# Performance work log

Measured on AMD Instinct MI355X. Metric: run time of the kernel, lower is better.

Reference implementation:

```python
import jax, jax.numpy as jnp
import numpy as np

GROUPS = 32
EPS = 1e-5
N_HEADS = 8


def setup_inputs() -> dict:
    key = jax.random.key(0)
    ks = jax.random.split(key, 12)
    B, H, W, C = 16, 64, 64, 512
    Nctx, Dctx = 77, 768
    s_c = 1.0 / np.sqrt(C)
    s_ctx = 1.0 / np.sqrt(Dctx)
    return {
        "x": jax.random.normal(ks[0], (B, H, W, C), jnp.float32),
        "context": jax.random.normal(ks[1], (B, Nctx, Dctx), jnp.float32),
        "gn_scale": jnp.ones((C,), jnp.float32),
        "gn_bias": jnp.zeros((C,), jnp.float32),
        "wq": jax.random.normal(ks[2], (C, C), jnp.float32) * s_c,
        "bq": jnp.zeros((C,), jnp.float32),
        "wk": jax.random.normal(ks[3], (Dctx, C), jnp.float32) * s_ctx,
        "bk": jnp.zeros((C,), jnp.float32),
        "wv": jax.random.normal(ks[4], (Dctx, C), jnp.float32) * s_ctx,
        "bv": jnp.zeros((C,), jnp.float32),
        "wo": jax.random.normal(ks[5], (C, C), jnp.float32) * s_c,
        "bo": jnp.zeros((C,), jnp.float32),
    }


def _group_norm(x, scale, bias):
    B, H, W, C = x.shape
    xg = x.reshape(B, H, W, GROUPS, C // GROUPS)
    mean = jnp.mean(xg, axis=(1, 2, 4), keepdims=True)
    var = jnp.var(xg, axis=(1, 2, 4), keepdims=True)
    xn = (xg - mean) * jax.lax.rsqrt(var + EPS)
    return xn.reshape(B, H, W, C) * scale + bias


def reference(x, context, gn_scale, gn_bias, wq, bq, wk, bk, wv, bv, wo, bo):
    B, H, W, C = x.shape
    head_dim = C // N_HEADS
    h = _group_norm(x, gn_scale, gn_bias)
    h_flat = h.reshape(B, H * W, C)
    Q = h_flat @ wq + bq                      # [B, N, C]
    K = context @ wk + bk                     # [B, Nctx, C]
    V = context @ wv + bv

    def split_heads(t):
        b, n, c = t.shape
        return t.reshape(b, n, N_HEADS, head_dim).transpose(0, 2, 1, 3)

    Qh, Kh, Vh = split_heads(Q), split_heads(K), split_heads(V)
    scale = 1.0 / jnp.sqrt(jnp.asarray(head_dim, x.dtype))
    scores = jnp.einsum('bhid,bhjd->bhij', Qh, Kh) * scale
    attn = jax.nn.softmax(scores, axis=-1)
    out = jnp.einsum('bhij,bhjd->bhid', attn, Vh)  # [B, h, N, d]
    out = out.transpose(0, 2, 1, 3).reshape(B, H * W, C)
    out = out @ wo + bo
    return out.reshape(B, H, W, C) + x
```

## Files before the change

### kernel.cpp

```cpp
#include <hip/hip_runtime.h>
#include <hip/hip_bf16.h>

typedef __attribute__((ext_vector_type(4))) float f32x4;
typedef __attribute__((ext_vector_type(8))) short bf16x8;
typedef unsigned short u16;

#define AS1 __attribute__((address_space(1)))
#define AS3 __attribute__((address_space(3)))

#define B_    16
#define HW_   4096
#define C_    512
#define NCTX  77
#define DCTX  768
#define NH    8
#define HD    64
#define EPSV  1e-5f

__device__ inline u16 f2bf(float f) {
    union { float f; unsigned u; } v; v.f = f;
    unsigned r = v.u + 0x7fffu + ((v.u >> 16) & 1u);
    return (u16)(r >> 16);
}
__device__ inline float bf2f(u16 h) {
    union { unsigned u; float f; } v; v.u = ((unsigned)h) << 16;
    return v.f;
}

__global__ __launch_bounds__(256) void gn_stats(const float* __restrict__ x,
                                                float* __restrict__ mean,
                                                float* __restrict__ rstd) {
    int b = blockIdx.x >> 5, g = blockIdx.x & 31;
    const float* px = x + (size_t)b * HW_ * C_ + g * 16;
    float s = 0.f, ss = 0.f;
    for (int t = threadIdx.x; t < HW_ * 4; t += 256) {
        int hw = t >> 2, c4 = (t & 3) * 4;
        const float4 v = *(const float4*)(px + (size_t)hw * C_ + c4);
        s  += v.x + v.y + v.z + v.w;
        ss += v.x * v.x + v.y * v.y + v.z * v.z + v.w * v.w;
    }
    for (int off = 32; off; off >>= 1) { s += __shfl_xor(s, off); ss += __shfl_xor(ss, off); }
    __shared__ float red[2][4];
    int wv = threadIdx.x >> 6, lane = threadIdx.x & 63;
    if (lane == 0) { red[0][wv] = s; red[1][wv] = ss; }
    __syncthreads();
    if (threadIdx.x == 0) {
        float S = red[0][0] + red[0][1] + red[0][2] + red[0][3];
        float SS = red[1][0] + red[1][1] + red[1][2] + red[1][3];
        float mn = S / 65536.f;
        float var = SS / 65536.f - mn * mn;
        mean[blockIdx.x] = mn;
        rstd[blockIdx.x] = rsqrtf(var + EPSV);
    }
}

__global__ __launch_bounds__(256) void transpose_cast(const float* __restrict__ src,
                                                      u16* __restrict__ dst, int K) {
    int idx = blockIdx.x * 256 + threadIdx.x;
    if (idx >= K * 512) return;
    int k = idx >> 9, n = idx & 511;
    dst[(size_t)n * K + k] = f2bf(src[idx]);
}

__global__ __launch_bounds__(256) void gemm_small(const float* __restrict__ A,
                                                  const u16* __restrict__ Bt,
                                                  const float* __restrict__ bias,
                                                  u16* __restrict__ out,
                                                  int M, int K) {
    __shared__ __align__(16) u16 As[128][40];
    __shared__ __align__(16) u16 Bs[128][40];
    int tid = threadIdx.x, lane = tid & 63, wid = tid >> 6;
    int wm = wid >> 1, wn = wid & 1;
    int row0 = blockIdx.y * 128, col0 = blockIdx.x * 128;
    int q = lane >> 4, r16 = lane & 15;

    f32x4 acc[4][4];
#pragma unroll
    for (int i = 0; i < 4; i++)
#pragma unroll
        for (int j = 0; j < 4; j++) acc[i][j] = (f32x4){0.f, 0.f, 0.f, 0.f};

    for (int k0 = 0; k0 < K; k0 += 32) {
#pragma unroll
        for (int it = 0; it < 2; ++it) {
            int e = it * 256 + tid;
            int rr = e >> 2, kc = (e & 3) * 8;
            int ga = row0 + rr; if (ga > M - 1) ga = M - 1;
            float4 a0 = *(const float4*)(A + (size_t)ga * K + k0 + kc);
            float4 a1 = *(const float4*)(A + (size_t)ga * K + k0 + kc + 4);
            bf16x8 av;
            av[0] = (short)f2bf(a0.x); av[1] = (short)f2bf(a0.y);
            av[2] = (short)f2bf(a0.z); av[3] = (short)f2bf(a0.w);
            av[4] = (short)f2bf(a1.x); av[5] = (short)f2bf(a1.y);
            av[6] = (short)f2bf(a1.z); av[7] = (short)f2bf(a1.w);
            *(bf16x8*)&As[rr][kc] = av;
            int gb = col0 + rr;
            bf16x8 bv = *(const bf16x8*)(Bt + (size_t)gb * K + k0 + kc);
            *(bf16x8*)&Bs[rr][kc] = bv;
        }
        __syncthreads();
        bf16x8 afr[4], bfr[4];
#pragma unroll
        for (int mi = 0; mi < 4; mi++) afr[mi] = *(const bf16x8*)&As[wm * 64 + mi * 16 + r16][q * 8];
#pragma unroll
        for (int ni = 0; ni < 4; ni++) bfr[ni] = *(const bf16x8*)&Bs[wn * 64 + ni * 16 + r16][q * 8];
#pragma unroll
        for (int mi = 0; mi < 4; mi++)
#pragma unroll
            for (int ni = 0; ni < 4; ni++)
                acc[mi][ni] = __builtin_amdgcn_mfma_f32_16x16x32_bf16(afr[mi], bfr[ni], acc[mi][ni], 0, 0, 0);
        __syncthreads();
    }

#pragma unroll
    for (int mi = 0; mi < 4; mi++) {
#pragma unroll
        for (int rr = 0; rr < 4; rr++) {
            int grow = row0 + wm * 64 + mi * 16 + q * 4 + rr;
            if (grow >= M) continue;
#pragma unroll
            for (int ni = 0; ni < 4; ni++) {
                int gcol = col0 + wn * 64 + ni * 16 + r16;
                float v = acc[mi][ni][rr] + bias[gcol];
                out[(size_t)grow * 512 + gcol] = f2bf(v);
            }
        }
    }
}

__global__ __launch_bounds__(256, 2) void gemm_fusedq(const float* __restrict__ x,
                                                      const float* __restrict__ mean,
                                                      const float* __restrict__ rstd,
                                                      const float* __restrict__ gns,
                                                      const float* __restrict__ gnb,
                                                      const u16* __restrict__ Bt,
                                                      const float* __restrict__ bias,
                                                      u16* __restrict__ out) {
    constexpr int K = 512;
    __shared__ __align__(16) u16 LA[2][8192];
    __shared__ __align__(16) u16 LB[2][8192];
    int tid = threadIdx.x, lane = tid & 63, wid = tid >> 6;
    int wr = wid >> 1, wc = wid & 1;
    int q = lane >> 4, r16 = lane & 15;

    int orig = blockIdx.x;
    int wg = (orig & 7) * 256 + (orig >> 3);
    int bx = wg & 3, by = wg >> 2;
    int row0 = by * 128, col0 = bx * 128;

    int srow = tid >> 3;
    int schunk = (tid & 7) ^ (srow & 7);
    const u16* gB = Bt + (size_t)(col0 + srow) * K + schunk * 8;
    const int lo = tid * 8;

    int c8 = tid & 7;
    int rbase = (tid >> 3) * 4;
    const float* xb = x + (size_t)(row0 + rbase) * 512 + c8 * 8;
    int bg0 = (row0 >> 12) * 32;

    f32x4 acc[4][4];
#pragma unroll
    for (int i = 0; i < 4; i++)
#pragma unroll
        for (int j = 0; j < 4; j++) acc[i][j] = (f32x4){0.f, 0.f, 0.f, 0.f};

    float4 ar[8];
    float mn, rs;
    float4 s0v, s1v, b0v, b1v;

#define LOADA(kt) do { _Pragma("unroll")                                          \
    for (int i_ = 0; i_ < 4; ++i_) {                                              \
        ar[2 * i_]     = *(const float4*)(xb + (kt) * 64 + (size_t)i_ * 512);     \
        ar[2 * i_ + 1] = *(const float4*)(xb + (kt) * 64 + (size_t)i_ * 512 + 4); \
    } } while (0)

#define LOADP(kt) do { int c0_ = (kt) * 64 + c8 * 8; int bg_ = bg0 + (c0_ >> 4);  \
    mn = mean[bg_]; rs = rstd[bg_];                                               \
    s0v = *(const float4*)(gns + c0_); s1v = *(const float4*)(gns + c0_ + 4);     \
    b0v = *(const float4*)(gnb + c0_); b1v = *(const float4*)(gnb + c0_ + 4);     \
  } while (0)

#define WRITEA(nbuf) do {                                                         \
    float m2_[8], a2_[8];                                                         \
    m2_[0]=rs*s0v.x; m2_[1]=rs*s0v.y; m2_[2]=rs*s0v.z; m2_[3]=rs*s0v.w;           \
    m2_[4]=rs*s1v.x; m2_[5]=rs*s1v.y; m2_[6]=rs*s1v.z; m2_[7]=rs*s1v.w;           \
    a2_[0]=b0v.x-mn*m2_[0]; a2_[1]=b0v.y-mn*m2_[1];                               \
    a2_[2]=b0v.z-mn*m2_[2]; a2_[3]=b0v.w-mn*m2_[3];                               \
    a2_[4]=b1v.x-mn*m2_[4]; a2_[5]=b1v.y-mn*m2_[5];                               \
    a2_[6]=b1v.z-mn*m2_[6]; a2_[7]=b1v.w-mn*m2_[7];                               \
    _Pragma("unroll")                                                             \
    for (int i_ = 0; i_ < 4; ++i_) {                                              \
        int row_ = rbase + i_;                                                    \
        bf16x8 pk_;                                                               \
        pk_[0]=(short)f2bf(ar[2*i_].x  *m2_[0]+a2_[0]);                           \
        pk_[1]=(short)f2bf(ar[2*i_].y  *m2_[1]+a2_[1]);                           \
        pk_[2]=(short)f2bf(ar[2*i_].z  *m2_[2]+a2_[2]);                           \
        pk_[3]=(short)f2bf(ar[2*i_].w  *m2_[3]+a2_[3]);                           \
        pk_[4]=(short)f2bf(ar[2*i_+1].x*m2_[4]+a2_[4]);                           \
        pk_[5]=(short)f2bf(ar[2*i_+1].y*m2_[5]+a2_[5]);                           \
        pk_[6]=(short)f2bf(ar[2*i_+1].z*m2_[6]+a2_[6]);                           \
        pk_[7]=(short)f2bf(ar[2*i_+1].w*m2_[7]+a2_[7]);                           \
        *(bf16x8*)&LA[nbuf][row_ * 64 + ((c8 ^ (row_ & 7)) * 8)] = pk_;           \
    } } while (0)

#define STG_B(kt, s) __builtin_amdgcn_global_load_lds( \
        (const AS1 void*)(gB + (kt) * 64 + (size_t)((s) * 32) * K), \
        (AS3 void*)(&LB[(kt) & 1][(s) * 2048 + lo]), 16, 0, 0)

#define PHASE_(buf, h, ks) do {                                                            \
    bf16x8 afr[2], bfr[4];                                                                 \
    const int ch_ = (((ks) * 4 + q) ^ (r16 & 7)) * 8;                                      \
    _Pragma("unroll")                                                                      \
    for (int mi = 0; mi < 2; mi++)                                                         \
        afr[mi] = *(const bf16x8*)&LA[buf][(wr * 64 + ((h) * 2 + mi) * 16 + r16) * 64 + ch_]; \
    _Pragma("unroll")                                                                      \
    for (int ni = 0; ni < 4; ni++)                                                         \
        bfr[ni] = *(const bf16x8*)&LB[buf][(wc * 64 + ni * 16 + r16) * 64 + ch_];          \
    __builtin_amdgcn_s_setprio(1);                                                         \
    _Pragma("unroll")                                                                      \
    for (int mi = 0; mi < 2; mi++)                                                         \
      _Pragma("unroll")                                                                    \
      for (int ni = 0; ni < 4; ni++)                                                       \
        acc[(h) * 2 + mi][ni] =                                                            \
            __builtin_amdgcn_mfma_f32_16x16x32_bf16(afr[mi], bfr[ni], acc[(h) * 2 + mi][ni], 0, 0, 0); \
    __builtin_amdgcn_s_setprio(0);                                                         \
  } while (0)

    LOADA(0); LOADP(0);
    asm volatile("" ::: "memory");
    STG_B(0, 0); STG_B(0, 1); STG_B(0, 2); STG_B(0, 3);
    asm volatile("s_waitcnt vmcnt(4)" ::: "memory");
    WRITEA(0);
    asm volatile("s_waitcnt lgkmcnt(0)" ::: "memory");

#pragma unroll
    for (int t = 0; t < 7; ++t) {
        const int buf = t & 1;
        LOADA(t + 1); LOADP(t + 1);
        asm volatile("" ::: "memory");
        STG_B(t + 1, 0); STG_B(t + 1, 1); STG_B(t + 1, 2); STG_B(t + 1, 3);
        asm volatile("s_waitcnt vmcnt(18)" ::: "memory");
        __builtin_amdgcn_s_barrier();
        asm volatile("" ::: "memory");
        PHASE_(buf, 0, 0); PHASE_(buf, 1, 0); PHASE_(buf, 0, 1); PHASE_(buf, 1, 1);
        asm volatile("s_waitcnt vmcnt(4)" ::: "memory");
        WRITEA(buf ^ 1);
        asm volatile("s_waitcnt lgkmcnt(0)" ::: "memory");
        __builtin_amdgcn_s_barrier();
        asm volatile("" ::: "memory");
    }
    asm volatile("s_waitcnt vmcnt(0) lgkmcnt(0)" ::: "memory");
    __builtin_amdgcn_s_barrier();
    asm volatile("" ::: "memory");
    PHASE_(1, 0, 0); PHASE_(1, 1, 0); PHASE_(1, 0, 1); PHASE_(1, 1, 1);
#undef LOADA
#undef LOADP
#undef WRITEA
#undef STG_B
#undef PHASE_

#pragma unroll
    for (int mi = 0; mi < 4; mi++) {
#pragma unroll
        for (int rr = 0; rr < 4; rr++) {
            int grow = row0 + wr * 64 + mi * 16 + q * 4 + rr;
#pragma unroll
            for (int ni = 0; ni < 4; ni++) {
                int gcol = col0 + wc * 64 + ni * 16 + r16;
                float v = acc[mi][ni][rr] + bias[gcol];
                out[(size_t)grow * 512 + gcol] = f2bf(v);
            }
        }
    }
}

__global__ __launch_bounds__(256, 4) void gemm_ring(const u16* __restrict__ A,
                                                    const u16* __restrict__ Bt,
                                                    const float* __restrict__ bias,
                                                    const float* __restrict__ res,
                                                    float* __restrict__ out) {
    constexpr int K = 512;
    __shared__ __align__(16) u16 LA[2][4096];
    __shared__ __align__(16) u16 LB[2][4096];
    int tid = threadIdx.x, lane = tid & 63, wid = tid >> 6;
    int wr = wid >> 1, wc = wid & 1;
    int q = lane >> 4, r16 = lane & 15;

    int orig = blockIdx.x;
    int wg = (orig & 7) * 256 + (orig >> 3);
    int bx = wg & 3, by = wg >> 2;
    int row0 = by * 128, col0 = bx * 128;

    int srow = tid >> 2;
    int schunk = (tid & 3) ^ (srow & 3);
    const u16* gA = A + (size_t)(row0 + srow) * K + schunk * 8;
    const u16* gB = Bt + (size_t)(col0 + srow) * K + schunk * 8;
    const int lo = tid * 8;

    f32x4 acc[4][4];
#pragma unroll
    for (int i = 0; i < 4; i++)
#pragma unroll
        for (int j = 0; j < 4; j++) acc[i][j] = (f32x4){0.f, 0.f, 0.f, 0.f};

#define STG(kt) do { int sl_ = (kt) & 1;                                              \
    __builtin_amdgcn_global_load_lds((const AS1 void*)(gA + (kt) * 32),               \
                                     (AS3 void*)(&LA[sl_][lo]), 16, 0, 0);            \
    __builtin_amdgcn_global_load_lds((const AS1 void*)(gA + (kt) * 32 + (size_t)64 * K), \
                                     (AS3 void*)(&LA[sl_][2048 + lo]), 16, 0, 0);     \
    __builtin_amdgcn_global_load_lds((const AS1 void*)(gB + (kt) * 32),               \
                                     (AS3 void*)(&LB[sl_][lo]), 16, 0, 0);            \
    __builtin_amdgcn_global_load_lds((const AS1 void*)(gB + (kt) * 32 + (size_t)64 * K), \
                                     (AS3 void*)(&LB[sl_][2048 + lo]), 16, 0, 0);     \
  } while (0)

#define COMPUTE(sl) do {                                                              \
    bf16x8 afr[4], bfr[4];                                                            \
    const int ch_ = (q ^ (r16 & 3)) * 8;                                              \
    _Pragma("unroll")                                                                 \
    for (int mi = 0; mi < 4; mi++)                                                    \
        afr[mi] = *(const bf16x8*)&LA[sl][(wr * 64 + mi * 16 + r16) * 32 + ch_];      \
    _Pragma("unroll")                                                                 \
    for (int ni = 0; ni < 4; ni++)                                                    \
        bfr[ni] = *(const bf16x8*)&LB[sl][(wc * 64 + ni * 16 + r16) * 32 + ch_];      \
    __builtin_amdgcn_s_setprio(1);                                                    \
    _Pragma("unroll")                                                                 \
    for (int mi = 0; mi < 4; mi++)                                                    \
      _Pragma("unroll")                                                               \
      for (int ni = 0; ni < 4; ni++)                                                  \
        acc[mi][ni] = __builtin_amdgcn_mfma_f32_16x16x32_bf16(afr[mi], bfr[ni], acc[mi][ni], 0, 0, 0); \
    __builtin_amdgcn_s_setprio(0);                                                    \
  } while (0)

    STG(0);
#pragma unroll
    for (int t = 0; t < 15; ++t) {
        STG(t + 1);
        asm volatile("s_waitcnt vmcnt(4)" ::: "memory");
        asm volatile("s_barrier" ::: "memory");
        COMPUTE(t & 1);
        asm volatile("s_barrier" ::: "memory");
    }
    asm volatile("s_waitcnt vmcnt(0)" ::: "memory");
    asm volatile("s_barrier" ::: "memory");
    COMPUTE(1);
#undef STG
#undef COMPUTE

#pragma unroll
    for (int mi = 0; mi < 4; mi++) {
#pragma unroll
        for (int rr = 0; rr < 4; rr++) {
            int grow = row0 + wr * 64 + mi * 16 + q * 4 + rr;
#pragma unroll
            for (int ni = 0; ni < 4; ni++) {
                int gcol = col0 + wc * 64 + ni * 16 + r16;
                float v = acc[mi][ni][rr] + bias[gcol];
                size_t idx = (size_t)grow * 512 + gcol;
                out[idx] = v + res[idx];
            }
        }
    }
}

__global__ __launch_bounds__(256) void attn_mfma(const u16* __restrict__ Qb,
                                                 const u16* __restrict__ Kb,
                                                 const u16* __restrict__ Vb,
                                                 u16* __restrict__ Ob) {
    __shared__ __align__(16) u16 Ks[80][72];
    __shared__ __align__(16) u16 VT[64][104];
    __shared__ __align__(16) u16 Ps[64][104];
    int tid = threadIdx.x, lane = tid & 63, wv = tid >> 6;
    int q = lane >> 4, r16 = lane & 15;
    int tile0 = blockIdx.x * 16;
    int bh = blockIdx.y;
    int b = bh >> 3, h = bh & 7;

    {
        unsigned* p0 = (unsigned*)&Ks[0][0];
        for (int i = tid; i < 2880; i += 256) p0[i] = 0u;
        unsigned* p1 = (unsigned*)&VT[0][0];
        for (int i = tid; i < 3328; i += 256) p1[i] = 0u;
        unsigned* p2 = (unsigned*)&Ps[0][0];
        for (int i = tid; i < 3328; i += 256) p2[i] = 0u;
    }
    __syncthreads();

    size_t kvbase = ((size_t)b * NCTX) * C_ + h * HD;
    for (int c = tid; c < NCTX * 8; c += 256) {
        int j = c >> 3, d8 = (c & 7) * 8;
        *(bf16x8*)&Ks[j][d8] = *(const bf16x8*)(Kb + kvbase + (size_t)j * C_ + d8);
    }
    for (int t = tid; t < NCTX * 64; t += 256) {
        int j = t >> 6, d = t & 63;
        VT[d][j] = Vb[kvbase + (size_t)j * C_ + d];
    }
    __syncthreads();

    const size_t tstep = (size_t)64 * C_;
    const u16* qp = Qb + ((size_t)b * HW_ + wv * 16 + r16) * C_ + h * HD + q * 8;
    bool v4 = (r16 < NCTX - 64);

    bf16x8 qc0 = *(const bf16x8*)(qp + (size_t)tile0 * tstep);
    bf16x8 qc1 = *(const bf16x8*)(qp + (size_t)tile0 * tstep + 32);

    for (int it = 0; it < 16; ++it) {
        int tile = tile0 + it;
        bf16x8 qn0 = qc0, qn1 = qc1;
        if (it < 15) {
            qn0 = *(const bf16x8*)(qp + (size_t)(tile + 1) * tstep);
            qn1 = *(const bf16x8*)(qp + (size_t)(tile + 1) * tstep + 32);
        }

        f32x4 accs[5];
#pragma unroll
        for (int nt = 0; nt < 5; ++nt) accs[nt] = (f32x4){0.f, 0.f, 0.f, 0.f};
#pragma unroll
        for (int nt = 0; nt < 5; ++nt) {
            bf16x8 kf = *(const bf16x8*)&Ks[nt * 16 + r16][q * 8];
            accs[nt] = __builtin_amdgcn_mfma_f32_16x16x32_bf16(qc0, kf, accs[nt], 0, 0, 0);
        }
#pragma unroll
        for (int nt = 0; nt < 5; ++nt) {
            bf16x8 kf = *(const bf16x8*)&Ks[nt * 16 + r16][32 + q * 8];
            accs[nt] = __builtin_amdgcn_mfma_f32_16x16x32_bf16(qc1, kf, accs[nt], 0, 0, 0);
        }

#pragma unroll
        for (int r = 0; r < 4; ++r) {
            float s[5];
#pragma unroll
            for (int nt = 0; nt < 5; ++nt) s[nt] = accs[nt][r] * 0.125f;
            float m = fmaxf(fmaxf(fmaxf(s[0], s[1]), fmaxf(s[2], s[3])), v4 ? s[4] : -3.0e38f);
#pragma unroll
            for (int off = 1; off < 16; off <<= 1) m = fmaxf(m, __shfl_xor(m, off));
            float e[5], sum = 0.f;
#pragma unroll
            for (int nt = 0; nt < 5; ++nt) {
                e[nt] = (nt < 4 || v4) ? __expf(s[nt] - m) : 0.f;
                sum += e[nt];
            }
#pragma unroll
            for (int off = 1; off < 16; off <<= 1) sum += __shfl_xor(sum, off);
            float inv = 1.0f / sum;
            int prow = wv * 16 + q * 4 + r;
#pragma unroll
            for (int nt = 0; nt < 5; ++nt)
                Ps[prow][nt * 16 + r16] = f2bf(e[nt] * inv);
        }

        f32x4 acco[4];
#pragma unroll
        for (int nt = 0; nt < 4; ++nt) acco[nt] = (f32x4){0.f, 0.f, 0.f, 0.f};
#pragma unroll
        for (int ks = 0; ks < 3; ++ks) {
            bf16x8 pf = *(const bf16x8*)&Ps[wv * 16 + r16][ks * 32 + q * 8];
#pragma unroll
            for (int nt = 0; nt < 4; ++nt) {
                bf16x8 vf = *(const bf16x8*)&VT[nt * 16 + r16][ks * 32 + q * 8];
                acco[nt] = __builtin_amdgcn_mfma_f32_16x16x32_bf16(pf, vf, acco[nt], 0, 0, 0);
            }
        }

        int row0 = tile * 64 + wv * 16;
#pragma unroll
        for (int nt = 0; nt < 4; ++nt)
#pragma unroll
            for (int r = 0; r < 4; ++r) {
                int row = row0 + q * 4 + r;
                int col = h * HD + nt * 16 + r16;
                Ob[((size_t)b * HW_ + row) * C_ + col] = f2bf(acco[nt][r]);
            }
        qc0 = qn0; qc1 = qn1;
    }
}

extern "C" void kernel_launch(void* const* d_in, const int* in_sizes, int n_in,
                              void* d_out, int out_size, void* d_ws, size_t ws_size,
                              hipStream_t stream) {
    const float* x   = (const float*)d_in[0];
    const float* ctx = (const float*)d_in[1];
    const float* gns = (const float*)d_in[2];
    const float* gnb = (const float*)d_in[3];
    const float* wq  = (const float*)d_in[4];
    const float* bq  = (const float*)d_in[5];
    const float* wk  = (const float*)d_in[6];
    const float* bk  = (const float*)d_in[7];
    const float* wv  = (const float*)d_in[8];
    const float* bv  = (const float*)d_in[9];
    const float* wo  = (const float*)d_in[10];
    const float* bo  = (const float*)d_in[11];

    char* ws = (char*)d_ws;
    float* mean = (float*)(ws + 0);
    float* rstd = (float*)(ws + 2048);
    u16* wqT  = (u16*)(ws + 4096);
    u16* wkT  = (u16*)(ws + 528384);
    u16* wvT  = (u16*)(ws + 1314816);
    u16* woT  = (u16*)(ws + 2101248);
    u16* aob  = (u16*)(ws + 4517888);
    u16* qb   = (u16*)(ws + 71626752);
    u16* kb   = (u16*)(ws + 138735616);
    u16* vb   = (u16*)(ws + 139997184);

    gn_stats<<<512, 256, 0, stream>>>(x, mean, rstd);
    transpose_cast<<<1024, 256, 0, stream>>>(wq, wqT, 512);
    transpose_cast<<<1536, 256, 0, stream>>>(wk, wkT, 768);
    transpose_cast<<<1536, 256, 0, stream>>>(wv, wvT, 768);
    transpose_cast<<<1024, 256, 0, stream>>>(wo, woT, 512);

    gemm_fusedq<<<2048, 256, 0, stream>>>(x, mean, rstd, gns, gnb, wqT, bq, qb);
    gemm_small<<<dim3(4, 10), 256, 0, stream>>>(ctx, wkT, bk, kb, 1232, 768);
    gemm_small<<<dim3(4, 10), 256, 0, stream>>>(ctx, wvT, bv, vb, 1232, 768);

    attn_mfma<<<dim3(4, 128), 256, 0, stream>>>(qb, kb, vb, aob);

    gemm_ring<<<2048, 256, 0, stream>>>(aob, woT, bo, x, (float*)d_out);
}
```

Baseline: 321.5 us.

## Merge weight transposes and K/V GEMMs into single launches; double attention grid

Folds the four weight transpose-cast launches into one kernel and the separate K and V projection GEMMs into one launch that picks K or V weights by block column. The attention kernel now processes 8 query tiles per block instead of 16, doubling the grid to 1024 blocks so more CUs have work. This cuts launch overhead and small-kernel tail time. In exchange, K/V staging into shared memory is repeated across twice as many blocks.

```diff
diff --git a/kernel.cpp b/kernel.cpp
--- a/kernel.cpp
+++ b/kernel.cpp
@@ -54,24 +54,50 @@
     }
 }
 
-__global__ __launch_bounds__(256) void transpose_cast(const float* __restrict__ src,
-                                                      u16* __restrict__ dst, int K) {
+__global__ __launch_bounds__(256) void transpose_all(const float* __restrict__ wq,
+                                                     const float* __restrict__ wk,
+                                                     const float* __restrict__ wv,
+                                                     const float* __restrict__ wo,
+                                                     u16* __restrict__ wqT,
+                                                     u16* __restrict__ wkT,
+                                                     u16* __restrict__ wvT,
+                                                     u16* __restrict__ woT) {
     int idx = blockIdx.x * 256 + threadIdx.x;
-    if (idx >= K * 512) return;
-    int k = idx >> 9, n = idx & 511;
-    dst[(size_t)n * K + k] = f2bf(src[idx]);
-}
-
-__global__ __launch_bounds__(256) void gemm_small(const float* __restrict__ A,
-                                                  const u16* __restrict__ Bt,
-                                                  const float* __restrict__ bias,
-                                                  u16* __restrict__ out,
-                                                  int M, int K) {
+    if (idx < 262144) {
+        int k = idx >> 9, n = idx & 511;
+        wqT[(size_t)n * 512 + k] = f2bf(wq[idx]);
+    } else if (idx < 655360) {
+        int i = idx - 262144;
+        int k = i >> 9, n = i & 511;
+        wkT[(size_t)n * 768 + k] = f2bf(wk[i]);
+    } else if (idx < 1048576) {
+        int i = idx - 655360;
+        int k = i >> 9, n = i & 511;
+        wvT[(size_t)n * 768 + k] = f2bf(wv[i]);
+    } else if (idx < 1310720) {
+        int i = idx - 1048576;
+        int k = i >> 9, n = i & 511;
+        woT[(size_t)n * 512 + k] = f2bf(wo[i]);
+    }
+}
+
+__global__ __launch_bounds__(256) void gemm_kv(const float* __restrict__ A,
+                                               const u16* __restrict__ wkT,
+                                               const u16* __restrict__ wvT,
+                                               const float* __restrict__ bk,
+                                               const float* __restrict__ bv,
+                                               u16* __restrict__ kb,
+                                               u16* __restrict__ vb) {
+    constexpr int M = 1232, K = 768;
     __shared__ __align__(16) u16 As[128][40];
     __shared__ __align__(16) u16 Bs[128][40];
+    int bx = blockIdx.x;
+    const u16* Bt = (bx < 4) ? wkT : wvT;
+    const float* bias = (bx < 4) ? bk : bv;
+    u16* out = (bx < 4) ? kb : vb;
     int tid = threadIdx.x, lane = tid & 63, wid = tid >> 6;
     int wm = wid >> 1, wn = wid & 1;
-    int row0 = blockIdx.y * 128, col0 = blockIdx.x * 128;
+    int row0 = blockIdx.y * 128, col0 = (bx & 3) * 128;
     int q = lane >> 4, r16 = lane & 15;
 
     f32x4 acc[4][4];
@@ -95,8 +121,8 @@
             av[6] = (short)f2bf(a1.z); av[7] = (short)f2bf(a1.w);
             *(bf16x8*)&As[rr][kc] = av;
             int gb = col0 + rr;
-            bf16x8 bv = *(const bf16x8*)(Bt + (size_t)gb * K + k0 + kc);
-            *(bf16x8*)&Bs[rr][kc] = bv;
+            bf16x8 bv8 = *(const bf16x8*)(Bt + (size_t)gb * K + k0 + kc);
+            *(bf16x8*)&Bs[rr][kc] = bv8;
         }
         __syncthreads();
         bf16x8 afr[4], bfr[4];
@@ -372,7 +398,7 @@
     __shared__ __align__(16) u16 Ps[64][104];
     int tid = threadIdx.x, lane = tid & 63, wv = tid >> 6;
     int q = lane >> 4, r16 = lane & 15;
-    int tile0 = blockIdx.x * 16;
+    int tile0 = blockIdx.x * 8;
     int bh = blockIdx.y;
     int b = bh >> 3, h = bh & 7;
 
@@ -404,10 +430,10 @@
     bf16x8 qc0 = *(const bf16x8*)(qp + (size_t)tile0 * tstep);
     bf16x8 qc1 = *(const bf16x8*)(qp + (size_t)tile0 * tstep + 32);
 
-    for (int it = 0; it < 16; ++it) {
+    for (int it = 0; it < 8; ++it) {
         int tile = tile0 + it;
         bf16x8 qn0 = qc0, qn1 = qc1;
-        if (it < 15) {
+        if (it < 7) {
             qn0 = *(const bf16x8*)(qp + (size_t)(tile + 1) * tstep);
             qn1 = *(const bf16x8*)(qp + (size_t)(tile + 1) * tstep + 32);
         }
@@ -504,16 +530,12 @@
     u16* vb   = (u16*)(ws + 139997184);
 
     gn_stats<<<512, 256, 0, stream>>>(x, mean, rstd);
-    transpose_cast<<<1024, 256, 0, stream>>>(wq, wqT, 512);
-    transpose_cast<<<1536, 256, 0, stream>>>(wk, wkT, 768);
-    transpose_cast<<<1536, 256, 0, stream>>>(wv, wvT, 768);
-    transpose_cast<<<1024, 256, 0, stream>>>(wo, woT, 512);
+    transpose_all<<<5120, 256, 0, stream>>>(wq, wk, wv, wo, wqT, wkT, wvT, woT);
 
     gemm_fusedq<<<2048, 256, 0, stream>>>(x, mean, rstd, gns, gnb, wqT, bq, qb);
-    gemm_small<<<dim3(4, 10), 256, 0, stream>>>(ctx, wkT, bk, kb, 1232, 768);
-    gemm_small<<<dim3(4, 10), 256, 0, stream>>>(ctx, wvT, bv, vb, 1232, 768);
-
-    attn_mfma<<<dim3(4, 128), 256, 0, stream>>>(qb, kb, vb, aob);
+    gemm_kv<<<dim3(8, 10), 256, 0, stream>>>(ctx, wkT, wvT, bk, bv, kb, vb);
+
+    attn_mfma<<<dim3(8, 128), 256, 0, stream>>>(qb, kb, vb, aob);
 
     gemm_ring<<<2048, 256, 0, stream>>>(aob, woT, bo, x, (float*)d_out);
 }
```

Measured after the change: 291.3 us. -9.4%, faster.
